# Performance work log

Hardware: AMD Instinct MI355X
Metric: run time of the kernel (lower is better)

## Reference

```python
import jax, jax.numpy as jnp
import numpy as np

N_NODES = 100000
N_EDGES = 1600000
D = 128          # fv_dim == num_hiddens == node_embed_dim
OUT_CH = 2
N_GIN = 3        # num_gin_layers (2) + final GINConv


def setup_inputs() -> dict:
    key = jax.random.key(0)
    ks = jax.random.split(key, 12)
    x = jax.random.normal(ks[0], (N_NODES, D), dtype=jnp.float32)
    src = jax.random.randint(ks[1], (N_EDGES,), 0, N_NODES, dtype=jnp.int32)
    dst = jax.random.randint(ks[2], (N_EDGES,), 0, N_NODES, dtype=jnp.int32)
    s = 0.05
    W1 = jax.random.normal(ks[3], (N_GIN, D, D), dtype=jnp.float32) * s
    b1 = jnp.zeros((N_GIN, D), dtype=jnp.float32)
    W2 = jax.random.normal(ks[4], (N_GIN, D, D), dtype=jnp.float32) * s
    b2 = jnp.zeros((N_GIN, D), dtype=jnp.float32)
    eps = jnp.zeros((N_GIN,), dtype=jnp.float32)  # learn_eps, init 0
    Wout = jax.random.normal(ks[5], (D, OUT_CH), dtype=jnp.float32) * s
    bout = jnp.zeros((OUT_CH,), dtype=jnp.float32)
    return {"x": x, "src": src, "dst": dst, "W1": W1, "b1": b1,
            "W2": W2, "b2": b2, "eps": eps, "Wout": Wout, "bout": bout}


def reference(x, src, dst, W1, b1, W2, b2, eps, Wout, bout):
    # in-degree for mean aggregation (clamped to 1, as DGL does for isolated nodes)
    deg = jax.ops.segment_sum(jnp.ones((N_EDGES,), x.dtype), dst,
                              num_segments=N_NODES)
    inv_deg = (1.0 / jnp.maximum(deg, 1.0))[:, None]  # [N,1]
    lrelu = jax.nn.leaky_relu  # torch default slope 0.01

    h = x
    for l in range(N_GIN):
        # GINConv, mean aggregator, learn_eps:
        # h' = MLP((1+eps) * h + mean_{j in N(i)} h_j)
        agg = jax.ops.segment_sum(h[src], dst, num_segments=N_NODES) * inv_deg
        z = (1.0 + eps[l]) * h + agg
        z = lrelu(z @ W1[l] + b1[l])      # Dropout(0.1) is identity in eval
        h = lrelu(z @ W2[l] + b2[l])
    n_embed = h                            # GIN.norm=False by default
    n_out = n_embed @ Wout + bout
    return (n_out, n_embed)
```

## Files before the change

### kernel.cpp

```cpp
#include <hip/hip_runtime.h>
#include <math.h>

#define N_NODES 100000
#define N_EDGES 1600000
#define D 128
#define SCAN_CHUNK 1024
#define N_SCAN_BLOCKS 98

typedef short short8_t __attribute__((ext_vector_type(8)));
typedef short short4_t __attribute__((ext_vector_type(4)));
typedef float floatx4 __attribute__((ext_vector_type(4)));

__device__ __forceinline__ unsigned short f32_to_bf16_rne(float f) {
  unsigned u = __builtin_bit_cast(unsigned, f);
  unsigned r = u + 0x7fffu + ((u >> 16) & 1u);
  return (unsigned short)(r >> 16);
}
__device__ __forceinline__ float bf16_bits_to_f32(unsigned short h) {
  return __builtin_bit_cast(float, (unsigned)h << 16);
}


__global__ __launch_bounds__(256) void k_count(const int* __restrict__ dst,
                                               int* __restrict__ counts) {
  int e = blockIdx.x * 256 + threadIdx.x;
  if (e < N_EDGES) atomicAdd(&counts[dst[e]], 1);
}

__global__ __launch_bounds__(256) void k_scan1(const int* __restrict__ counts,
                                               int* __restrict__ bsum) {
  __shared__ int red[256];
  int base = blockIdx.x * SCAN_CHUNK + threadIdx.x * 4;
  int s = 0;
#pragma unroll
  for (int j = 0; j < 4; j++) {
    int i = base + j;
    s += (i < N_NODES) ? counts[i] : 0;
  }
  red[threadIdx.x] = s;
  __syncthreads();
  for (int off = 128; off > 0; off >>= 1) {
    if (threadIdx.x < off) red[threadIdx.x] += red[threadIdx.x + off];
    __syncthreads();
  }
  if (threadIdx.x == 0) bsum[blockIdx.x] = red[0];
}

__global__ void k_scan2(const int* __restrict__ bsum, int* __restrict__ boff,
                        int* __restrict__ row_ptr, int nb) {
  if (threadIdx.x == 0) {
    int run = 0;
    for (int i = 0; i < nb; i++) { boff[i] = run; run += bsum[i]; }
    row_ptr[N_NODES] = run;
  }
}

__global__ __launch_bounds__(256) void k_scan3(const int* __restrict__ counts,
                                               const int* __restrict__ boff,
                                               int* __restrict__ row_ptr,
                                               int* __restrict__ cursor,
                                               float* __restrict__ inv_deg) {
  __shared__ int sd[256];
  int base = blockIdx.x * SCAN_CHUNK + threadIdx.x * 4;
  int c[4];
  int s = 0;
#pragma unroll
  for (int j = 0; j < 4; j++) {
    int i = base + j;
    c[j] = (i < N_NODES) ? counts[i] : 0;
    s += c[j];
  }
  sd[threadIdx.x] = s;
  __syncthreads();
  for (int off = 1; off < 256; off <<= 1) {
    int add = (threadIdx.x >= off) ? sd[threadIdx.x - off] : 0;
    __syncthreads();
    sd[threadIdx.x] += add;
    __syncthreads();
  }
  int excl = (threadIdx.x ? sd[threadIdx.x - 1] : 0) + boff[blockIdx.x];
#pragma unroll
  for (int j = 0; j < 4; j++) {
    int i = base + j;
    if (i < N_NODES) {
      row_ptr[i] = excl;
      cursor[i] = excl;
      inv_deg[i] = 1.0f / fmaxf((float)c[j], 1.0f);
      excl += c[j];
    }
  }
}

__global__ __launch_bounds__(256) void k_scatter(const int* __restrict__ src,
                                                 const int* __restrict__ dst,
                                                 int* __restrict__ cursor,
                                                 int* __restrict__ ssrc) {
  int e = blockIdx.x * 256 + threadIdx.x;
  if (e < N_EDGES) {
    int pos = atomicAdd(&cursor[dst[e]], 1);
    ssrc[pos] = src[e];
  }
}

__global__ __launch_bounds__(256) void k_agg(const float* __restrict__ h,
                                             float* __restrict__ z,
                                             const int* __restrict__ row_ptr,
                                             const int* __restrict__ ssrc,
                                             const float* __restrict__ inv_deg,
                                             const float* __restrict__ eps,
                                             int layer) {
  int node = blockIdx.x * 4 + (threadIdx.x >> 6);
  int t = threadIdx.x & 63;
  int beg = row_ptr[node];
  int end = row_ptr[node + 1];
  const float* hp = h + 2 * t;
  float ax0 = 0.f, ay0 = 0.f, ax1 = 0.f, ay1 = 0.f;
  float ax2 = 0.f, ay2 = 0.f, ax3 = 0.f, ay3 = 0.f;
  int e = beg;
  for (; e + 4 <= end; e += 4) {
    int i0 = ssrc[e + 0];
    int i1 = ssrc[e + 1];
    int i2 = ssrc[e + 2];
    int i3 = ssrc[e + 3];
    float2 v0 = *(const float2*)(hp + (size_t)i0 * D);
    float2 v1 = *(const float2*)(hp + (size_t)i1 * D);
    float2 v2 = *(const float2*)(hp + (size_t)i2 * D);
    float2 v3 = *(const float2*)(hp + (size_t)i3 * D);
    ax0 += v0.x; ay0 += v0.y;
    ax1 += v1.x; ay1 += v1.y;
    ax2 += v2.x; ay2 += v2.y;
    ax3 += v3.x; ay3 += v3.y;
  }
  for (; e < end; ++e) {
    int i = ssrc[e];
    float2 v = *(const float2*)(hp + (size_t)i * D);
    ax0 += v.x; ay0 += v.y;
  }
  float sx = (ax0 + ax1) + (ax2 + ax3);
  float sy = (ay0 + ay1) + (ay2 + ay3);
  float2 hv = *(const float2*)(hp + (size_t)node * D);
  float ep1 = 1.0f + eps[layer];
  float id = inv_deg[node];
  float2 o;
  o.x = ep1 * hv.x + sx * id;
  o.y = ep1 * hv.y + sy * id;
  *(float2*)(z + (size_t)node * D + 2 * t) = o;
}

__global__ __launch_bounds__(256) void k_wprep(const float* __restrict__ W1,
                                               const float* __restrict__ W2,
                                               short* __restrict__ WT) {
  int mat = blockIdx.y;
  const float* Wsrc = (mat < 3) ? (W1 + (size_t)mat * D * D)
                                : (W2 + (size_t)(mat - 3) * D * D);
  int idx = blockIdx.x * 256 + threadIdx.x;
  int k = idx >> 7;
  int c = idx & 127;
  float f = Wsrc[idx];
  unsigned short hi = f32_to_bf16_rne(f);
  float lo_f = f - bf16_bits_to_f32(hi);
  unsigned short lo = f32_to_bf16_rne(lo_f);
  short* base = WT + (size_t)mat * 2 * 16384;
  base[c * 128 + k] = (short)hi;
  base[16384 + c * 128 + k] = (short)lo;
}

#define LDS_STRIDE 40
__global__ __launch_bounds__(256, 2) void k_gemm(const float* __restrict__ A,
                                                 const short* __restrict__ WhT,
                                                 const short* __restrict__ WlT,
                                                 const float* __restrict__ bias,
                                                 float* __restrict__ C, int nrows) {
  __shared__ short Ah[128 * LDS_STRIDE];
  __shared__ short Al[128 * LDS_STRIDE];
  __shared__ short Wh[128 * LDS_STRIDE];
  __shared__ short Wl[128 * LDS_STRIDE];

  const int tid = threadIdx.x;
  const int row0 = blockIdx.x * 128;
  const int wave = tid >> 6;
  const int lane = tid & 63;
  const int wr = wave >> 1;
  const int wc = wave & 1;
  const int lr = lane & 15;
  const int koff = lane >> 4;

  floatx4 acc[4][4];
#pragma unroll
  for (int i = 0; i < 4; i++)
#pragma unroll
    for (int j = 0; j < 4; j++) acc[i][j] = (floatx4)(0.f);

  const int sr = tid >> 1;
  const int skq = tid & 1;
  int arow = row0 + sr;
  if (arow >= nrows) arow = nrows - 1;
  const float* Arow = A + (size_t)arow * D;
  const int swc = tid >> 1;
  const int skh = tid & 1;

  for (int k0 = 0; k0 < 128; k0 += 32) {
#pragma unroll
    for (int j = 0; j < 4; j++) {
      float4 av = *(const float4*)(Arow + k0 + skq * 16 + 4 * j);
      float f[4] = {av.x, av.y, av.z, av.w};
      short4_t hi4, lo4;
#pragma unroll
      for (int q = 0; q < 4; q++) {
        unsigned short h = f32_to_bf16_rne(f[q]);
        float lf = f[q] - bf16_bits_to_f32(h);
        hi4[q] = (short)h;
        lo4[q] = (short)f32_to_bf16_rne(lf);
      }
      *(short4_t*)&Ah[sr * LDS_STRIDE + skq * 16 + 4 * j] = hi4;
      *(short4_t*)&Al[sr * LDS_STRIDE + skq * 16 + 4 * j] = lo4;
    }
    {
      const short* ph = WhT + swc * 128 + k0 + skh * 16;
      const short* pl = WlT + swc * 128 + k0 + skh * 16;
      short8_t h0 = *(const short8_t*)(ph);
      short8_t h1 = *(const short8_t*)(ph + 8);
      short8_t l0 = *(const short8_t*)(pl);
      short8_t l1 = *(const short8_t*)(pl + 8);
      *(short8_t*)&Wh[swc * LDS_STRIDE + skh * 16] = h0;
      *(short8_t*)&Wh[swc * LDS_STRIDE + skh * 16 + 8] = h1;
      *(short8_t*)&Wl[swc * LDS_STRIDE + skh * 16] = l0;
      *(short8_t*)&Wl[swc * LDS_STRIDE + skh * 16 + 8] = l1;
    }
    __syncthreads();

    short8_t ah[4], al[4], wh[4], wl[4];
#pragma unroll
    for (int i = 0; i < 4; i++) {
      int r = wr * 64 + i * 16 + lr;
      ah[i] = *(const short8_t*)&Ah[r * LDS_STRIDE + koff * 8];
      al[i] = *(const short8_t*)&Al[r * LDS_STRIDE + koff * 8];
    }
#pragma unroll
    for (int j = 0; j < 4; j++) {
      int c = wc * 64 + j * 16 + lr;
      wh[j] = *(const short8_t*)&Wh[c * LDS_STRIDE + koff * 8];
      wl[j] = *(const short8_t*)&Wl[c * LDS_STRIDE + koff * 8];
    }
#pragma unroll
    for (int i = 0; i < 4; i++)
#pragma unroll
      for (int j = 0; j < 4; j++) {
        acc[i][j] = __builtin_amdgcn_mfma_f32_16x16x32_bf16(ah[i], wh[j], acc[i][j], 0, 0, 0);
        acc[i][j] = __builtin_amdgcn_mfma_f32_16x16x32_bf16(ah[i], wl[j], acc[i][j], 0, 0, 0);
        acc[i][j] = __builtin_amdgcn_mfma_f32_16x16x32_bf16(al[i], wh[j], acc[i][j], 0, 0, 0);
      }
    __syncthreads();
  }

  float bj[4];
#pragma unroll
  for (int j = 0; j < 4; j++) bj[j] = bias[wc * 64 + j * 16 + lr];
#pragma unroll
  for (int i = 0; i < 4; i++) {
#pragma unroll
    for (int r = 0; r < 4; r++) {
      int row = row0 + wr * 64 + i * 16 + koff * 4 + r;
      if (row < nrows) {
#pragma unroll
        for (int j = 0; j < 4; j++) {
          int col = wc * 64 + j * 16 + lr;
          float v = acc[i][j][r] + bj[j];
          v = v > 0.f ? v : 0.01f * v;
          C[(size_t)row * D + col] = v;
        }
      }
    }
  }
}

__global__ __launch_bounds__(256) void k_out(const float* __restrict__ h,
                                             const float* __restrict__ Wout,
                                             const float* __restrict__ bout,
                                             float* __restrict__ out) {
  int node = blockIdx.x * 4 + (threadIdx.x >> 6);
  int lane = threadIdx.x & 63;
  float2 hv = *(const float2*)(h + (size_t)node * D + lane * 2);
  float4 wv = *(const float4*)(Wout + lane * 4);
  float p0 = hv.x * wv.x + hv.y * wv.z;
  float p1 = hv.x * wv.y + hv.y * wv.w;
#pragma unroll
  for (int off = 32; off > 0; off >>= 1) {
    p0 += __shfl_down(p0, off, 64);
    p1 += __shfl_down(p1, off, 64);
  }
  if (lane == 0) {
    out[node * 2 + 0] = p0 + bout[0];
    out[node * 2 + 1] = p1 + bout[1];
  }
}


extern "C" void kernel_launch(void* const* d_in, const int* in_sizes, int n_in,
                              void* d_out, int out_size, void* d_ws, size_t ws_size,
                              hipStream_t stream) {
  const float* x = (const float*)d_in[0];
  const int* src = (const int*)d_in[1];
  const int* dst = (const int*)d_in[2];
  const float* W1 = (const float*)d_in[3];
  const float* b1 = (const float*)d_in[4];
  const float* W2 = (const float*)d_in[5];
  const float* b2 = (const float*)d_in[6];
  const float* eps = (const float*)d_in[7];
  const float* Wout = (const float*)d_in[8];
  const float* bout = (const float*)d_in[9];
  float* out = (float*)d_out;
  float* n_embed = out + (size_t)2 * N_NODES;

  char* ws = (char*)d_ws;
  size_t off = 0;
  auto alloc = [&](size_t bytes) -> char* {
    char* p = ws + off;
    off += (bytes + 511) & ~(size_t)511;
    return p;
  };
  float* bufA = (float*)alloc(sizeof(float) * (size_t)N_NODES * D);
  int* counts = (int*)alloc(sizeof(int) * N_NODES);
  int* row_ptr = (int*)alloc(sizeof(int) * (N_NODES + 1));
  int* cursor = (int*)alloc(sizeof(int) * N_NODES);
  float* inv_deg = (float*)alloc(sizeof(float) * N_NODES);
  int* bsum = (int*)alloc(sizeof(int) * 128);
  int* boff = (int*)alloc(sizeof(int) * 128);
  int* ssrc = (int*)alloc(sizeof(int) * N_EDGES);
  short* WT = (short*)alloc(sizeof(short) * 6 * 2 * 16384);

  hipMemsetAsync(counts, 0, sizeof(int) * N_NODES, stream);
  k_count<<<N_EDGES / 256, 256, 0, stream>>>(dst, counts);
  k_scan1<<<N_SCAN_BLOCKS, 256, 0, stream>>>(counts, bsum);
  k_scan2<<<1, 64, 0, stream>>>(bsum, boff, row_ptr, N_SCAN_BLOCKS);
  k_scan3<<<N_SCAN_BLOCKS, 256, 0, stream>>>(counts, boff, row_ptr, cursor, inv_deg);
  k_scatter<<<N_EDGES / 256, 256, 0, stream>>>(src, dst, cursor, ssrc);

  k_wprep<<<dim3(64, 6), 256, 0, stream>>>(W1, W2, WT);

  const int gemm_grid = (N_NODES + 127) / 128;
  const float* hin = x;
  float* t0 = bufA;
  float* t1 = n_embed;
  for (int l = 0; l < 3; l++) {
    float* za = (l % 2 == 0) ? t1 : t0;
    float* zb = (l % 2 == 0) ? t0 : t1;
    const short* w1h = WT + (size_t)l * 2 * 16384;
    const short* w1l = w1h + 16384;
    const short* w2h = WT + (size_t)(3 + l) * 2 * 16384;
    const short* w2l = w2h + 16384;
    k_agg<<<N_NODES / 4, 256, 0, stream>>>(hin, za, row_ptr, ssrc, inv_deg, eps, l);
    k_gemm<<<gemm_grid, 256, 0, stream>>>(za, w1h, w1l, b1 + (size_t)l * D, zb, N_NODES);
    k_gemm<<<gemm_grid, 256, 0, stream>>>(zb, w2h, w2l, b2 + (size_t)l * D, za, N_NODES);
    hin = za;
  }
  k_out<<<N_NODES / 4, 256, 0, stream>>>(n_embed, Wout, bout, out);
}
```

Baseline: 815.8 us.

## Build CSR via bucketed partition sort and pass activations as bf16 hi/lo planes

The per-edge global atomic scatter that builds the CSR source list is replaced by two passes. The first partitions edges into 1024-node buckets through LDS staging with one global atomic per bucket per block. The second sorts each bucket with LDS atomics, so global writes are more local. Separately, the aggregation and first GEMM now write activations as precomputed bf16 hi/lo split planes, so the GEMM loads them directly instead of converting fp32 to split-bf16 in its inner loop. This adds two launches and an intermediate edge buffer, aliased onto the z planes, and the first GEMM now reads and writes the same planes in place.

```diff
diff --git a/kernel.cpp b/kernel.cpp
--- a/kernel.cpp
+++ b/kernel.cpp
@@ -6,9 +6,12 @@
 #define D 128
 #define SCAN_CHUNK 1024
 #define N_SCAN_BLOCKS 98
+#define N_BUCKETS 98
+#define EDGES_PER_PART 4096
+#define N_PART_BLOCKS ((N_EDGES + EDGES_PER_PART - 1) / EDGES_PER_PART)
 
 typedef short short8_t __attribute__((ext_vector_type(8)));
-typedef short short4_t __attribute__((ext_vector_type(4)));
+typedef short short2_t __attribute__((ext_vector_type(2)));
 typedef float floatx4 __attribute__((ext_vector_type(4)));
 
 __device__ __forceinline__ unsigned short f32_to_bf16_rne(float f) {
@@ -58,7 +61,6 @@
 __global__ __launch_bounds__(256) void k_scan3(const int* __restrict__ counts,
                                                const int* __restrict__ boff,
                                                int* __restrict__ row_ptr,
-                                               int* __restrict__ cursor,
                                                float* __restrict__ inv_deg) {
   __shared__ int sd[256];
   int base = blockIdx.x * SCAN_CHUNK + threadIdx.x * 4;
@@ -84,26 +86,96 @@
     int i = base + j;
     if (i < N_NODES) {
       row_ptr[i] = excl;
-      cursor[i] = excl;
       inv_deg[i] = 1.0f / fmaxf((float)c[j], 1.0f);
       excl += c[j];
     }
   }
 }
 
-__global__ __launch_bounds__(256) void k_scatter(const int* __restrict__ src,
-                                                 const int* __restrict__ dst,
-                                                 int* __restrict__ cursor,
-                                                 int* __restrict__ ssrc) {
-  int e = blockIdx.x * 256 + threadIdx.x;
-  if (e < N_EDGES) {
-    int pos = atomicAdd(&cursor[dst[e]], 1);
-    ssrc[pos] = src[e];
+__global__ void k_binit(const int* __restrict__ row_ptr,
+                        int* __restrict__ bucket_cursor) {
+  int t = threadIdx.x;
+  if (t < N_BUCKETS) bucket_cursor[t] = row_ptr[t << 10];
+}
+
+__global__ __launch_bounds__(1024) void k_part(const int* __restrict__ src,
+                                               const int* __restrict__ dst,
+                                               int* __restrict__ bucket_cursor,
+                                               int2* __restrict__ ebuf) {
+  __shared__ int2 eLDS[EDGES_PER_PART];
+  __shared__ int hist[N_BUCKETS];
+  __shared__ int lbase[N_BUCKETS];
+  __shared__ int lcur[N_BUCKETS];
+  __shared__ int gbase[N_BUCKETS];
+  const int t = threadIdx.x;
+  const int base = blockIdx.x * EDGES_PER_PART;
+  const int count = min(EDGES_PER_PART, N_EDGES - base);
+  if (t < N_BUCKETS) hist[t] = 0;
+  __syncthreads();
+  int s[4], d[4];
+#pragma unroll
+  for (int j = 0; j < 4; j++) {
+    int local = j * 1024 + t;
+    if (local < count) {
+      s[j] = src[base + local];
+      d[j] = dst[base + local];
+      atomicAdd(&hist[d[j] >> 10], 1);
+    } else {
+      d[j] = -1;
+    }
+  }
+  __syncthreads();
+  if (t == 0) {
+    int run = 0;
+    for (int b = 0; b < N_BUCKETS; b++) { lbase[b] = run; run += hist[b]; }
+  }
+  __syncthreads();
+  if (t < N_BUCKETS) {
+    lcur[t] = lbase[t];
+    gbase[t] = hist[t] ? atomicAdd(&bucket_cursor[t], hist[t]) : 0;
+  }
+  __syncthreads();
+#pragma unroll
+  for (int j = 0; j < 4; j++) {
+    if (d[j] >= 0) {
+      int p = atomicAdd(&lcur[d[j] >> 10], 1);
+      eLDS[p] = make_int2(s[j], d[j]);
+    }
+  }
+  __syncthreads();
+#pragma unroll
+  for (int j = 0; j < 4; j++) {
+    int slot = j * 1024 + t;
+    if (slot < count) {
+      int2 e = eLDS[slot];
+      int b = e.y >> 10;
+      ebuf[gbase[b] + (slot - lbase[b])] = e;
+    }
+  }
+}
+
+__global__ __launch_bounds__(1024) void k_lsort(const int2* __restrict__ ebuf,
+                                                const int* __restrict__ row_ptr,
+                                                int* __restrict__ ssrc) {
+  __shared__ int lcur[1024];
+  const int b = blockIdx.x;
+  const int t = threadIdx.x;
+  const int node_base = b << 10;
+  const int nb = min(1024, N_NODES - node_base);
+  if (t < nb) lcur[t] = row_ptr[node_base + t];
+  __syncthreads();
+  const int rbeg = row_ptr[node_base];
+  const int rend = row_ptr[node_base + nb];
+  for (int i = rbeg + t; i < rend; i += 1024) {
+    int2 e = ebuf[i];
+    int p = atomicAdd(&lcur[e.y - node_base], 1);
+    ssrc[p] = e.x;
   }
 }
 
 __global__ __launch_bounds__(256) void k_agg(const float* __restrict__ h,
-                                             float* __restrict__ z,
+                                             short* __restrict__ zh,
+                                             short* __restrict__ zl,
                                              const int* __restrict__ row_ptr,
                                              const int* __restrict__ ssrc,
                                              const float* __restrict__ inv_deg,
@@ -141,10 +213,17 @@
   float2 hv = *(const float2*)(hp + (size_t)node * D);
   float ep1 = 1.0f + eps[layer];
   float id = inv_deg[node];
-  float2 o;
-  o.x = ep1 * hv.x + sx * id;
-  o.y = ep1 * hv.y + sy * id;
-  *(float2*)(z + (size_t)node * D + 2 * t) = o;
+  float zx = ep1 * hv.x + sx * id;
+  float zy = ep1 * hv.y + sy * id;
+  unsigned short hx = f32_to_bf16_rne(zx);
+  unsigned short hy = f32_to_bf16_rne(zy);
+  unsigned short lx = f32_to_bf16_rne(zx - bf16_bits_to_f32(hx));
+  unsigned short ly = f32_to_bf16_rne(zy - bf16_bits_to_f32(hy));
+  short2_t hw, lw;
+  hw[0] = (short)hx; hw[1] = (short)hy;
+  lw[0] = (short)lx; lw[1] = (short)ly;
+  *(short2_t*)&zh[(size_t)node * D + 2 * t] = hw;
+  *(short2_t*)&zl[(size_t)node * D + 2 * t] = lw;
 }
 
 __global__ __launch_bounds__(256) void k_wprep(const float* __restrict__ W1,
@@ -166,11 +245,15 @@
 }
 
 #define LDS_STRIDE 40
-__global__ __launch_bounds__(256, 2) void k_gemm(const float* __restrict__ A,
+__global__ __launch_bounds__(256, 2) void k_gemm(const short* __restrict__ Aph,
+                                                 const short* __restrict__ Apl,
                                                  const short* __restrict__ WhT,
                                                  const short* __restrict__ WlT,
                                                  const float* __restrict__ bias,
-                                                 float* __restrict__ C, int nrows) {
+                                                 float* __restrict__ Cf,
+                                                 short* __restrict__ Cph,
+                                                 short* __restrict__ Cpl,
+                                                 int nrows, int plane_out) {
   __shared__ short Ah[128 * LDS_STRIDE];
   __shared__ short Al[128 * LDS_STRIDE];
   __shared__ short Wh[128 * LDS_STRIDE];
@@ -191,42 +274,32 @@
 #pragma unroll
     for (int j = 0; j < 4; j++) acc[i][j] = (floatx4)(0.f);
 
-  const int sr = tid >> 1;
-  const int skq = tid & 1;
-  int arow = row0 + sr;
+  const int rs = tid >> 1;
+  const int sa = (tid & 1) * 16;
+  int arow = row0 + rs;
   if (arow >= nrows) arow = nrows - 1;
-  const float* Arow = A + (size_t)arow * D;
-  const int swc = tid >> 1;
-  const int skh = tid & 1;
+  const short* pAh = Aph + (size_t)arow * D;
+  const short* pAl = Apl + (size_t)arow * D;
+  const short* pWh = WhT + (size_t)rs * D;
+  const short* pWl = WlT + (size_t)rs * D;
 
   for (int k0 = 0; k0 < 128; k0 += 32) {
-#pragma unroll
-    for (int j = 0; j < 4; j++) {
-      float4 av = *(const float4*)(Arow + k0 + skq * 16 + 4 * j);
-      float f[4] = {av.x, av.y, av.z, av.w};
-      short4_t hi4, lo4;
-#pragma unroll
-      for (int q = 0; q < 4; q++) {
-        unsigned short h = f32_to_bf16_rne(f[q]);
-        float lf = f[q] - bf16_bits_to_f32(h);
-        hi4[q] = (short)h;
-        lo4[q] = (short)f32_to_bf16_rne(lf);
-      }
-      *(short4_t*)&Ah[sr * LDS_STRIDE + skq * 16 + 4 * j] = hi4;
-      *(short4_t*)&Al[sr * LDS_STRIDE + skq * 16 + 4 * j] = lo4;
-    }
-    {
-      const short* ph = WhT + swc * 128 + k0 + skh * 16;
-      const short* pl = WlT + swc * 128 + k0 + skh * 16;
-      short8_t h0 = *(const short8_t*)(ph);
-      short8_t h1 = *(const short8_t*)(ph + 8);
-      short8_t l0 = *(const short8_t*)(pl);
-      short8_t l1 = *(const short8_t*)(pl + 8);
-      *(short8_t*)&Wh[swc * LDS_STRIDE + skh * 16] = h0;
-      *(short8_t*)&Wh[swc * LDS_STRIDE + skh * 16 + 8] = h1;
-      *(short8_t*)&Wl[swc * LDS_STRIDE + skh * 16] = l0;
-      *(short8_t*)&Wl[swc * LDS_STRIDE + skh * 16 + 8] = l1;
-    }
+    short8_t a0 = *(const short8_t*)(pAh + k0 + sa);
+    short8_t a1 = *(const short8_t*)(pAh + k0 + sa + 8);
+    short8_t b0 = *(const short8_t*)(pAl + k0 + sa);
+    short8_t b1 = *(const short8_t*)(pAl + k0 + sa + 8);
+    short8_t w0 = *(const short8_t*)(pWh + k0 + sa);
+    short8_t w1 = *(const short8_t*)(pWh + k0 + sa + 8);
+    short8_t x0 = *(const short8_t*)(pWl + k0 + sa);
+    short8_t x1 = *(const short8_t*)(pWl + k0 + sa + 8);
+    *(short8_t*)&Ah[rs * LDS_STRIDE + sa] = a0;
+    *(short8_t*)&Ah[rs * LDS_STRIDE + sa + 8] = a1;
+    *(short8_t*)&Al[rs * LDS_STRIDE + sa] = b0;
+    *(short8_t*)&Al[rs * LDS_STRIDE + sa + 8] = b1;
+    *(short8_t*)&Wh[rs * LDS_STRIDE + sa] = w0;
+    *(short8_t*)&Wh[rs * LDS_STRIDE + sa + 8] = w1;
+    *(short8_t*)&Wl[rs * LDS_STRIDE + sa] = x0;
+    *(short8_t*)&Wl[rs * LDS_STRIDE + sa + 8] = x1;
     __syncthreads();
 
     short8_t ah[4], al[4], wh[4], wl[4];
@@ -256,18 +329,40 @@
   float bj[4];
 #pragma unroll
   for (int j = 0; j < 4; j++) bj[j] = bias[wc * 64 + j * 16 + lr];
-#pragma unroll
-  for (int i = 0; i < 4; i++) {
-#pragma unroll
-    for (int r = 0; r < 4; r++) {
-      int row = row0 + wr * 64 + i * 16 + koff * 4 + r;
-      if (row < nrows) {
-#pragma unroll
-        for (int j = 0; j < 4; j++) {
-          int col = wc * 64 + j * 16 + lr;
-          float v = acc[i][j][r] + bj[j];
-          v = v > 0.f ? v : 0.01f * v;
-          C[(size_t)row * D + col] = v;
+  if (plane_out) {
+#pragma unroll
+    for (int i = 0; i < 4; i++) {
+#pragma unroll
+      for (int r = 0; r < 4; r++) {
+        int row = row0 + wr * 64 + i * 16 + koff * 4 + r;
+        if (row < nrows) {
+#pragma unroll
+          for (int j = 0; j < 4; j++) {
+            int col = wc * 64 + j * 16 + lr;
+            float v = acc[i][j][r] + bj[j];
+            v = v > 0.f ? v : 0.01f * v;
+            unsigned short hv = f32_to_bf16_rne(v);
+            unsigned short lv = f32_to_bf16_rne(v - bf16_bits_to_f32(hv));
+            Cph[(size_t)row * D + col] = (short)hv;
+            Cpl[(size_t)row * D + col] = (short)lv;
+          }
+        }
+      }
+    }
+  } else {
+#pragma unroll
+    for (int i = 0; i < 4; i++) {
+#pragma unroll
+      for (int r = 0; r < 4; r++) {
+        int row = row0 + wr * 64 + i * 16 + koff * 4 + r;
+        if (row < nrows) {
+#pragma unroll
+          for (int j = 0; j < 4; j++) {
+            int col = wc * 64 + j * 16 + lr;
+            float v = acc[i][j][r] + bj[j];
+            v = v > 0.f ? v : 0.01f * v;
+            Cf[(size_t)row * D + col] = v;
+          }
         }
       }
     }
@@ -319,40 +414,42 @@
     off += (bytes + 511) & ~(size_t)511;
     return p;
   };
-  float* bufA = (float*)alloc(sizeof(float) * (size_t)N_NODES * D);
+  short* zh = (short*)alloc(sizeof(short) * (size_t)N_NODES * D);
+  short* zl = (short*)alloc(sizeof(short) * (size_t)N_NODES * D);
+  int* ssrc = (int*)alloc(sizeof(int) * N_EDGES);
   int* counts = (int*)alloc(sizeof(int) * N_NODES);
   int* row_ptr = (int*)alloc(sizeof(int) * (N_NODES + 1));
-  int* cursor = (int*)alloc(sizeof(int) * N_NODES);
   float* inv_deg = (float*)alloc(sizeof(float) * N_NODES);
   int* bsum = (int*)alloc(sizeof(int) * 128);
   int* boff = (int*)alloc(sizeof(int) * 128);
-  int* ssrc = (int*)alloc(sizeof(int) * N_EDGES);
+  int* bucket_cursor = (int*)alloc(sizeof(int) * 128);
   short* WT = (short*)alloc(sizeof(short) * 6 * 2 * 16384);
+  int2* ebuf = (int2*)zh;
 
   hipMemsetAsync(counts, 0, sizeof(int) * N_NODES, stream);
   k_count<<<N_EDGES / 256, 256, 0, stream>>>(dst, counts);
   k_scan1<<<N_SCAN_BLOCKS, 256, 0, stream>>>(counts, bsum);
   k_scan2<<<1, 64, 0, stream>>>(bsum, boff, row_ptr, N_SCAN_BLOCKS);
-  k_scan3<<<N_SCAN_BLOCKS, 256, 0, stream>>>(counts, boff, row_ptr, cursor, inv_deg);
-  k_scatter<<<N_EDGES / 256, 256, 0, stream>>>(src, dst, cursor, ssrc);
+  k_scan3<<<N_SCAN_BLOCKS, 256, 0, stream>>>(counts, boff, row_ptr, inv_deg);
+  k_binit<<<1, 128, 0, stream>>>(row_ptr, bucket_cursor);
+  k_part<<<N_PART_BLOCKS, 1024, 0, stream>>>(src, dst, bucket_cursor, ebuf);
+  k_lsort<<<N_BUCKETS, 1024, 0, stream>>>(ebuf, row_ptr, ssrc);
 
   k_wprep<<<dim3(64, 6), 256, 0, stream>>>(W1, W2, WT);
 
   const int gemm_grid = (N_NODES + 127) / 128;
-  const float* hin = x;
-  float* t0 = bufA;
-  float* t1 = n_embed;
   for (int l = 0; l < 3; l++) {
-    float* za = (l % 2 == 0) ? t1 : t0;
-    float* zb = (l % 2 == 0) ? t0 : t1;
+    const float* hin = (l == 0) ? x : n_embed;
     const short* w1h = WT + (size_t)l * 2 * 16384;
     const short* w1l = w1h + 16384;
     const short* w2h = WT + (size_t)(3 + l) * 2 * 16384;
     const short* w2l = w2h + 16384;
-    k_agg<<<N_NODES / 4, 256, 0, stream>>>(hin, za, row_ptr, ssrc, inv_deg, eps, l);
-    k_gemm<<<gemm_grid, 256, 0, stream>>>(za, w1h, w1l, b1 + (size_t)l * D, zb, N_NODES);
-    k_gemm<<<gemm_grid, 256, 0, stream>>>(zb, w2h, w2l, b2 + (size_t)l * D, za, N_NODES);
-    hin = za;
+    k_agg<<<N_NODES / 4, 256, 0, stream>>>(hin, zh, zl, row_ptr, ssrc, inv_deg, eps, l);
+    k_gemm<<<gemm_grid, 256, 0, stream>>>(zh, zl, w1h, w1l, b1 + (size_t)l * D,
+                                          (float*)nullptr, zh, zl, N_NODES, 1);
+    k_gemm<<<gemm_grid, 256, 0, stream>>>(zh, zl, w2h, w2l, b2 + (size_t)l * D,
+                                          n_embed, (short*)nullptr, (short*)nullptr,
+                                          N_NODES, 0);
   }
   k_out<<<N_NODES / 4, 256, 0, stream>>>(n_embed, Wout, bout, out);
 }
```

New measurement: 752.3 us. 7.8% less time.
